# Optimization experiments

Measured on AMD Instinct MI355X. Metric: run time of the kernel, lower is better.

## Reference

```python
import jax, jax.numpy as jnp
import numpy as np

TOPK_RATIO = 0.2
DICE_WEIGHT = 0.5
SHAPE = (2, 1, 128, 192, 192)


def setup_inputs() -> dict:
    key = jax.random.key(0)
    k1, k2 = jax.random.split(key)
    logits = jax.random.normal(k1, SHAPE, dtype=jnp.float32)
    targets = jax.random.uniform(k2, SHAPE, dtype=jnp.float32)
    return {"logits": logits, "targets": targets}


def _bce_with_logits(x, t):
    # stable: max(x,0) - x*t + log(1+exp(-|x|))
    return jnp.maximum(x, 0.0) - x * t + jnp.log1p(jnp.exp(-jnp.abs(x)))


def reference(logits, targets):
    # --- TopK BCE ---
    flat_loss = _bce_with_logits(logits, targets).reshape(-1)
    n = flat_loss.shape[0]
    k_samples = max(1, int(n * TOPK_RATIO))
    topk_losses, _ = jax.lax.top_k(flat_loss, k_samples)
    bce = jnp.mean(topk_losses)

    # --- Soft Dice ---
    p = jax.nn.sigmoid(logits).reshape(-1)
    t = targets.reshape(-1)
    intersection = jnp.sum(p * t)
    union = jnp.sum(p) + jnp.sum(t)
    dice = (2.0 * intersection + 1e-06) / (union + 1e-06)
    dice_loss = 1.0 - dice

    return bce + DICE_WEIGHT * dice_loss
```

## Files before the change

### kernel.cpp

```cpp
#include <hip/hip_runtime.h>
#include <math.h>
#include <limits.h>

#define NB1 8192
#define NB2 4096
#define VEC 4

__device__ unsigned g_H1[NB1];
__device__ unsigned g_hist2[NB2];
__device__ float    g_band[2];
__device__ unsigned g_done1 = 0;

__device__ __forceinline__ void elem_f(float x, float t, float& l, float& p) {
    float e = __expf(-fabsf(x));
    l = fmaxf(x, 0.f) - x * t + __logf(1.f + e);
    float r = __builtin_amdgcn_rcpf(1.f + e);
    p = (x >= 0.f) ? r : e * r;
}

__global__ __launch_bounds__(256) void sample_band_kernel(
    const float4* __restrict__ x4, const float4* __restrict__ t4,
    int n4, long long ks, long long M)
{
    __shared__ unsigned lh[NB1];
    __shared__ int is_last;
    for (int i = threadIdx.x; i < NB1; i += 256) lh[i] = 0u;
    __syncthreads();

    int nth = gridDim.x * 256;
    int tid = blockIdx.x * 256 + threadIdx.x;
    int S4 = n4 >> 4;
    int i0 = tid, i1 = tid + nth;

    float4 xa, ta, xb, tb;
    bool v0 = i0 < S4, v1 = i1 < S4;
    if (v0) {
        int f4 = ((i0 >> 6) << 10) + (i0 & 63);
        xa = x4[f4]; ta = t4[f4];
    }
    if (v1) {
        int f4 = ((i1 >> 6) << 10) + (i1 & 63);
        xb = x4[f4]; tb = t4[f4];
    }
    if (v0) {
        float xs[4] = {xa.x, xa.y, xa.z, xa.w};
        float ts[4] = {ta.x, ta.y, ta.z, ta.w};
        #pragma unroll
        for (int c = 0; c < 4; ++c) {
            float l, p; elem_f(xs[c], ts[c], l, p);
            atomicAdd(&lh[__float_as_uint(l) >> 19], 1u);
        }
    }
    if (v1) {
        float xs[4] = {xb.x, xb.y, xb.z, xb.w};
        float ts[4] = {tb.x, tb.y, tb.z, tb.w};
        #pragma unroll
        for (int c = 0; c < 4; ++c) {
            float l, p; elem_f(xs[c], ts[c], l, p);
            atomicAdd(&lh[__float_as_uint(l) >> 19], 1u);
        }
    }
    __syncthreads();
    for (int i = threadIdx.x; i < NB1; i += 256) {
        unsigned c = lh[i];
        if (c) atomicAdd(&g_H1[i], c);
    }
    __syncthreads();

    if (threadIdx.x == 0) {
        __threadfence();
        is_last = (atomicAdd(&g_done1, 1u) == (unsigned)(gridDim.x - 1));
    }
    __syncthreads();
    if (!is_last) return;
    __threadfence();

    const uint4* hv = (const uint4*)g_H1;
    uint4* lv = (uint4*)lh;
    for (int i = threadIdx.x; i < NB1 / 4; i += 256) lv[i] = hv[i];
    __syncthreads();
    for (int i = threadIdx.x; i < NB1; i += 256) g_H1[i] = 0u;
    if (threadIdx.x == 0) g_done1 = 0u;

    if (threadIdx.x < 64) {
        int lane = threadIdx.x;
        int base = lane << 7;
        unsigned long long chunk = 0;
        for (int j = 0; j < 128; ++j) chunk += lh[base + j];
        unsigned long long s = chunk;
        #pragma unroll
        for (int off = 1; off < 64; off <<= 1) {
            unsigned long long v = __shfl_down(s, off);
            if (lane + off < 64) s += v;
        }
        unsigned long long above = s - chunk;

        int my_bhi = INT_MAX, my_blo = -1;
        unsigned long long c = above;
        for (int j = 127; j >= 0; --j) {
            unsigned h = lh[base + j];
            if ((long long)(c + h) < ks - M) my_bhi = base + j;
            if ((long long)c > ks + M && my_blo < 0) my_blo = base + j;
            c += h;
        }
        #pragma unroll
        for (int off = 32; off; off >>= 1) {
            int a = __shfl_down(my_bhi, off); my_bhi = min(my_bhi, a);
            int b = __shfl_down(my_blo, off); my_blo = max(my_blo, b);
        }
        if (lane == 0) {
            int bhi = (my_bhi == INT_MAX) ? (NB1 - 1) : my_bhi;
            int blo = my_blo;
            float vhi = __uint_as_float((unsigned)bhi << 19);
            float vlo = (blo < 0) ? 0.f : __uint_as_float((unsigned)(blo + 1) << 19);
            if (!(vlo < vhi)) vlo = 0.f;
            g_band[0] = vlo;
            g_band[1] = vhi;
        }
    }
}

__device__ __forceinline__ void process4(
    float4 xv, float4 tv, float vlo, float vhi, float scale,
    float& sp, float& spt, float& st, float& sgt, unsigned& cnt)
{
    float xs[4] = {xv.x, xv.y, xv.z, xv.w};
    float ts[4] = {tv.x, tv.y, tv.z, tv.w};
    #pragma unroll
    for (int c = 0; c < 4; ++c) {
        float l, p;
        elem_f(xs[c], ts[c], l, p);
        sp += p; spt += p * ts[c]; st += ts[c];
        if (l >= vhi) { cnt++; sgt += l; }
        else if (l >= vlo) {
            int b = min((int)((l - vlo) * scale), NB2 - 1);
            atomicAdd(&g_hist2[b], 1u);
        }
    }
}

__global__ __launch_bounds__(256, 4) void main_kernel(
    const float4* __restrict__ x4, const float4* __restrict__ t4,
    float* __restrict__ q0, float* __restrict__ q1,
    float* __restrict__ q2, float* __restrict__ q3, unsigned* __restrict__ qc,
    const float* __restrict__ xg, const float* __restrict__ tg,
    int n, int n4)
{
    float vlo = g_band[0], vhi = g_band[1];
    float scale = (float)NB2 / (vhi - vlo);

    int base = blockIdx.x * (256 * VEC) + threadIdx.x;
    float sp = 0.f, spt = 0.f, st = 0.f, sgt = 0.f;
    unsigned cnt = 0;

    bool full = (blockIdx.x + 1) * (256 * VEC) <= n4;
    if (full) {
        float4 xv[VEC], tv[VEC];
        #pragma unroll
        for (int j = 0; j < VEC; ++j) xv[j] = x4[base + j * 256];
        #pragma unroll
        for (int j = 0; j < VEC; ++j) tv[j] = t4[base + j * 256];
        #pragma unroll
        for (int j = 0; j < VEC; ++j)
            process4(xv[j], tv[j], vlo, vhi, scale, sp, spt, st, sgt, cnt);
    } else {
        for (int j = 0; j < VEC; ++j) {
            int idx = base + j * 256;
            if (idx < n4)
                process4(x4[idx], t4[idx], vlo, vhi, scale, sp, spt, st, sgt, cnt);
        }
    }
    int tail0 = n4 << 2;
    if (blockIdx.x == 0 && threadIdx.x < (n - tail0)) {
        float x = xg[tail0 + threadIdx.x], t = tg[tail0 + threadIdx.x];
        float l, p;
        elem_f(x, t, l, p);
        sp += p; spt += p * t; st += t;
        if (l >= vhi) { cnt++; sgt += l; }
        else if (l >= vlo) {
            int b = min((int)((l - vlo) * scale), NB2 - 1);
            atomicAdd(&g_hist2[b], 1u);
        }
    }

    #pragma unroll
    for (int off = 32; off; off >>= 1) {
        sp  += __shfl_down(sp,  off);
        spt += __shfl_down(spt, off);
        st  += __shfl_down(st,  off);
        sgt += __shfl_down(sgt, off);
        cnt += __shfl_down(cnt, off);
    }
    __shared__ float    rs[4][4];
    __shared__ unsigned rc[4];
    int w = threadIdx.x >> 6;
    if ((threadIdx.x & 63) == 0) {
        rs[w][0] = sp; rs[w][1] = spt; rs[w][2] = st; rs[w][3] = sgt; rc[w] = cnt;
    }
    __syncthreads();
    if (threadIdx.x == 0) {
        float a0 = 0, a1 = 0, a2 = 0, a3 = 0;
        unsigned c = 0;
        #pragma unroll
        for (int i = 0; i < 4; ++i) {
            a0 += rs[i][0]; a1 += rs[i][1]; a2 += rs[i][2]; a3 += rs[i][3]; c += rc[i];
        }
        q0[blockIdx.x] = a0; q1[blockIdx.x] = a1; q2[blockIdx.x] = a2;
        q3[blockIdx.x] = a3; qc[blockIdx.x] = c;
    }
}

__global__ __launch_bounds__(1024) void final_kernel(
    const float* __restrict__ q0, const float* __restrict__ q1,
    const float* __restrict__ q2, const float* __restrict__ q3,
    const unsigned* __restrict__ qc, int nblocks,
    float* __restrict__ out, long long k)
{
    __shared__ unsigned lh[NB2];
    __shared__ double red[16][5];
    __shared__ double fin[5];

    for (int i = threadIdx.x; i < NB2; i += 1024) {
        lh[i] = g_hist2[i];
        g_hist2[i] = 0u;
    }

    double a0 = 0, a1 = 0, a2 = 0, a3 = 0, a4 = 0;
    for (int i = threadIdx.x; i < nblocks; i += 1024) {
        a0 += (double)q0[i]; a1 += (double)q1[i]; a2 += (double)q2[i];
        a3 += (double)q3[i]; a4 += (double)qc[i];
    }
    #pragma unroll
    for (int off = 32; off; off >>= 1) {
        a0 += __shfl_down(a0, off); a1 += __shfl_down(a1, off);
        a2 += __shfl_down(a2, off); a3 += __shfl_down(a3, off);
        a4 += __shfl_down(a4, off);
    }
    int w = threadIdx.x >> 6;
    if ((threadIdx.x & 63) == 0) {
        red[w][0] = a0; red[w][1] = a1; red[w][2] = a2; red[w][3] = a3; red[w][4] = a4;
    }
    __syncthreads();
    if (threadIdx.x == 0) {
        double f0 = 0, f1 = 0, f2 = 0, f3 = 0, f4 = 0;
        for (int i = 0; i < 16; ++i) {
            f0 += red[i][0]; f1 += red[i][1]; f2 += red[i][2];
            f3 += red[i][3]; f4 += red[i][4];
        }
        fin[0] = f0; fin[1] = f1; fin[2] = f2; fin[3] = f3; fin[4] = f4;
    }
    __syncthreads();
    if (threadIdx.x >= 64) return;

    int lane = threadIdx.x;
    double SP = fin[0], SPT = fin[1], ST = fin[2], SGT = fin[3];
    long long CNT = (long long)fin[4];

    double vlo = (double)g_band[0], vhi = (double)g_band[1];
    double binw = (vhi - vlo) / NB2;
    long long k2 = k - CNT;

    int base = lane << 6;
    unsigned long long cchunk = 0;
    double wchunk = 0.0;
    for (int j = 0; j < 64; ++j) {
        unsigned h = lh[base + j];
        cchunk += h;
        wchunk += (double)h * (vlo + (base + j + 0.5) * binw);
    }
    unsigned long long cs = cchunk;
    double wsum = wchunk;
    #pragma unroll
    for (int off = 1; off < 64; off <<= 1) {
        unsigned long long cv = __shfl_down(cs, off);
        double wv = __shfl_down(wsum, off);
        if (lane + off < 64) { cs += cv; wsum += wv; }
    }
    unsigned long long total = __shfl(cs, 0);
    double wtotal = __shfl(wsum, 0);

    double I = SPT, U = SP + ST;
    double dice_part = 0.5 * (1.0 - (2.0 * I + 1e-6) / (U + 1e-6));

    if (k2 <= 0) {
        if (lane == 0) out[0] = (float)(SGT / (double)k + dice_part);
        return;
    }
    if ((unsigned long long)k2 > total) {
        if (lane == 0) {
            double sum_top = SGT + wtotal + (double)(k2 - (long long)total) * vlo;
            out[0] = (float)(sum_top / (double)k + dice_part);
        }
        return;
    }
    unsigned long long c = cs - cchunk;
    double wacc = wsum - wchunk;
    for (int j = 63; j >= 0; --j) {
        unsigned h = lh[base + j];
        double val = vlo + (base + j + 0.5) * binw;
        if (c < (unsigned long long)k2 && (unsigned long long)k2 <= c + h) {
            double sum_top = SGT + wacc + (double)((long long)k2 - (long long)c) * val;
            out[0] = (float)(sum_top / (double)k + dice_part);
        }
        c += h;
        wacc += (double)h * val;
    }
}

extern "C" void kernel_launch(void* const* d_in, const int* in_sizes, int n_in,
                              void* d_out, int out_size, void* d_ws, size_t ws_size,
                              hipStream_t stream)
{
    const float* x = (const float*)d_in[0];
    const float* t = (const float*)d_in[1];
    float* out = (float*)d_out;
    int n = in_sizes[0];
    int n4 = n >> 2;
    long long k = (long long)((double)n * 0.2);
    if (k < 1) k = 1;

    long long S = (long long)(n4 >> 4) * 4;
    long long ks = (S > 0) ? (long long)((double)k * (double)S / (double)n) : 0;
    long long M = 4096;

    int tilesz = 256 * VEC;
    int grid = (n4 + tilesz - 1) / tilesz;
    if (grid < 1) grid = 1;

    int S4 = n4 >> 4;
    int sgrid = (S4 + 511) / 512;
    if (sgrid < 1) sgrid = 1;

    unsigned char* ws = (unsigned char*)d_ws;
    size_t pstride = (((size_t)grid * 4) + 255) & ~(size_t)255;
    float*    q0 = (float*)(ws);
    float*    q1 = (float*)(ws + pstride);
    float*    q2 = (float*)(ws + 2 * pstride);
    float*    q3 = (float*)(ws + 3 * pstride);
    unsigned* qc = (unsigned*)(ws + 4 * pstride);

    sample_band_kernel<<<sgrid, 256, 0, stream>>>((const float4*)x, (const float4*)t,
                                                  n4, ks, M);
    main_kernel<<<grid, 256, 0, stream>>>((const float4*)x, (const float4*)t,
                                          q0, q1, q2, q3, qc, x, t, n, n4);
    final_kernel<<<1, 1024, 0, stream>>>(q0, q1, q2, q3, qc, grid, out, k);
}
```

Measured before the change: 140.3 us.

## Make main kernel persistent grid-stride with double-buffered register prefetch

Replaces the one-tile-per-block main kernel with a fixed grid of persistent blocks that loop over tiles in grid-stride order. Each block prefetches the next tile into a second register buffer while it processes the current one, so load latency overlaps with compute. This also cuts the number of per-block partial sums that the final kernel reduces. In exchange it roughly doubles register pressure per thread and relies on a fixed grid size, which could leave CUs underused or lower occupancy.

```diff
diff --git a/kernel.cpp b/kernel.cpp
--- a/kernel.cpp
+++ b/kernel.cpp
@@ -4,7 +4,8 @@
 
 #define NB1 8192
 #define NB2 4096
-#define VEC 4
+#define TV 4
+#define GRID_MAIN 768
 
 __device__ unsigned g_H1[NB1];
 __device__ unsigned g_hist2[NB2];
@@ -149,30 +150,72 @@
     float vlo = g_band[0], vhi = g_band[1];
     float scale = (float)NB2 / (vhi - vlo);
 
-    int base = blockIdx.x * (256 * VEC) + threadIdx.x;
+    int ntiles = (n4 + 1023) >> 10;
+    int fullTiles = n4 >> 10;
+    int tid = threadIdx.x;
+
     float sp = 0.f, spt = 0.f, st = 0.f, sgt = 0.f;
     unsigned cnt = 0;
 
-    bool full = (blockIdx.x + 1) * (256 * VEC) <= n4;
-    if (full) {
-        float4 xv[VEC], tv[VEC];
-        #pragma unroll
-        for (int j = 0; j < VEC; ++j) xv[j] = x4[base + j * 256];
-        #pragma unroll
-        for (int j = 0; j < VEC; ++j) tv[j] = t4[base + j * 256];
-        #pragma unroll
-        for (int j = 0; j < VEC; ++j)
-            process4(xv[j], tv[j], vlo, vhi, scale, sp, spt, st, sgt, cnt);
-    } else {
-        for (int j = 0; j < VEC; ++j) {
-            int idx = base + j * 256;
-            if (idx < n4)
-                process4(x4[idx], t4[idx], vlo, vhi, scale, sp, spt, st, sgt, cnt);
-        }
-    }
+    float4 xa[TV], ta[TV], xb[TV], tb[TV];
+
+    auto LOAD = [&](int tile, float4 (&xd)[TV], float4 (&td)[TV]) {
+        int base = (tile << 10) + tid;
+        if (tile < fullTiles) {
+            #pragma unroll
+            for (int j = 0; j < TV; ++j) xd[j] = x4[base + j * 256];
+            #pragma unroll
+            for (int j = 0; j < TV; ++j) td[j] = t4[base + j * 256];
+        } else {
+            #pragma unroll
+            for (int j = 0; j < TV; ++j) {
+                int idx = base + j * 256;
+                if (idx < n4) { xd[j] = x4[idx]; td[j] = t4[idx]; }
+            }
+        }
+    };
+    auto COMP = [&](int tile, float4 (&xd)[TV], float4 (&td)[TV]) {
+        if (tile < fullTiles) {
+            #pragma unroll
+            for (int j = 0; j < TV; ++j)
+                process4(xd[j], td[j], vlo, vhi, scale, sp, spt, st, sgt, cnt);
+        } else {
+            int base = (tile << 10) + tid;
+            #pragma unroll
+            for (int j = 0; j < TV; ++j) {
+                int idx = base + j * 256;
+                if (idx < n4)
+                    process4(xd[j], td[j], vlo, vhi, scale, sp, spt, st, sgt, cnt);
+            }
+        }
+    };
+
+    int t0 = blockIdx.x;
+    if (t0 < ntiles) {
+        LOAD(t0, xa, ta);
+        while (true) {
+            int t1 = t0 + GRID_MAIN;
+            if (t1 < ntiles) {
+                LOAD(t1, xb, tb);
+                COMP(t0, xa, ta);
+                int t2 = t1 + GRID_MAIN;
+                if (t2 < ntiles) {
+                    LOAD(t2, xa, ta);
+                    COMP(t1, xb, tb);
+                    t0 = t2;
+                    continue;
+                }
+                COMP(t1, xb, tb);
+                break;
+            }
+            COMP(t0, xa, ta);
+            break;
+        }
+    }
+
     int tail0 = n4 << 2;
-    if (blockIdx.x == 0 && threadIdx.x < (n - tail0)) {
-        float x = xg[tail0 + threadIdx.x], t = tg[tail0 + threadIdx.x];
+    if (blockIdx.x == 0 && tid < (n - tail0)) {
+        float x = xg[tail0 + tid], t = tg[tail0 + tid];
         float l, p;
         elem_f(x, t, l, p);
         sp += p; spt += p * t; st += t;
@@ -193,12 +236,12 @@
     }
     __shared__ float    rs[4][4];
     __shared__ unsigned rc[4];
-    int w = threadIdx.x >> 6;
-    if ((threadIdx.x & 63) == 0) {
+    int w = tid >> 6;
+    if ((tid & 63) == 0) {
         rs[w][0] = sp; rs[w][1] = spt; rs[w][2] = st; rs[w][3] = sgt; rc[w] = cnt;
     }
     __syncthreads();
-    if (threadIdx.x == 0) {
+    if (tid == 0) {
         float a0 = 0, a1 = 0, a2 = 0, a3 = 0;
         unsigned c = 0;
         #pragma unroll
@@ -323,9 +366,7 @@
     long long ks = (S > 0) ? (long long)((double)k * (double)S / (double)n) : 0;
     long long M = 4096;
 
-    int tilesz = 256 * VEC;
-    int grid = (n4 + tilesz - 1) / tilesz;
-    if (grid < 1) grid = 1;
+    int grid = GRID_MAIN;
 
     int S4 = n4 >> 4;
     int sgrid = (S4 + 511) / 512;
```

New measurement: 141.6 us. Within noise of the previous version (+0.9%).
